# Optimization experiments

Measured on AMD Instinct MI355X. Metric: run time of the kernel, lower is better.

The kernel has to match this reference:

```python
import jax, jax.numpy as jnp
import numpy as np

# Hardcoded 6-node part graph from the module (src, dst) pairs; PyG flows src->dst.
_EDGES = np.array([[0,1],[0,2],[0,3],[0,4],[0,5],[1,2],[1,3],[1,4],[1,5],[2,3],[2,4],[3,5],[4,5],[1,0],[2,0],[3,0],[4,0],[5,0],[2,1],[3,1],[4,1],[5,1],[3,2],[4,2],[5,3],[5,4]], dtype=np.int32)
SRC = jnp.asarray(_EDGES[:, 0])
DST = jnp.asarray(_EDGES[:, 1])
NUM_NODES = 6


def setup_inputs() -> dict:
    key = jax.random.key(0)
    k0, k1, k2 = jax.random.split(key, 3)
    C, B = 128, 32768
    x = jax.random.normal(k0, (NUM_NODES, B, C), dtype=jnp.float32)
    # SAGEConv weights: lin_l (aggregated neighbors, carries bias) and lin_r (root)
    W_l = jax.random.normal(k1, (2 * C, C), dtype=jnp.float32) / np.sqrt(C).astype(np.float32)
    W_r = jax.random.normal(k2, (2 * C, C), dtype=jnp.float32) / np.sqrt(C).astype(np.float32)
    b = jnp.zeros((2 * C,), dtype=jnp.float32)
    return {"x": x, "W_l": W_l, "W_r": W_r, "b": b}


def reference(x, W_l, W_r, b):
    # x: [N=6, B, C]
    # mean aggregation of source features at each destination node
    msg = x[SRC]                                                  # [E, B, C]
    agg = jax.ops.segment_sum(msg, DST, num_segments=NUM_NODES)   # [N, B, C]
    deg = jax.ops.segment_sum(jnp.ones_like(DST, dtype=x.dtype), DST, num_segments=NUM_NODES)
    agg = agg / deg[:, None, None]
    # SAGEConv: lin_l(agg) + lin_r(x), bias in lin_l
    y = jnp.einsum('nbc,oc->nbo', agg, W_l) + b + jnp.einsum('nbc,oc->nbo', x, W_r)
    y = jax.nn.gelu(y, approximate=False)                         # torch F.gelu = exact erf
    # Python cat-loop over nodes == concatenate the 6 node slices along features
    N, B, O = y.shape
    return jnp.transpose(y, (1, 0, 2)).reshape(B, N * O)          # [B, 6*2C]
```

## Files before the change

kernel.cpp:

```cpp
#include <hip/hip_runtime.h>
#include <hip/hip_bf16.h>

#define NB 32768
#define CD 128
#define NNODES 6
#define OUTW 1536
#define GPB 8
#define NBLK (NB / 16 / GPB)

#define PW_P  0
#define PW_M0 32768
#define PW_M2 65536
#define PW_N  98304

typedef __attribute__((ext_vector_type(8))) short short8;
typedef __attribute__((ext_vector_type(4))) short s16x4;
typedef __attribute__((ext_vector_type(4))) float f32x4;

static __device__ __forceinline__ short f2bf(float f) {
    union { __bf16 b; short s; } u;
    u.b = (__bf16)f;
    return u.s;
}

static __device__ __forceinline__ short8 pack8(f32x4 a, f32x4 b) {
    short8 p;
    #pragma unroll
    for (int j = 0; j < 4; ++j) { p[j] = f2bf(a[j]); p[4 + j] = f2bf(b[j]); }
    return p;
}

static __device__ __forceinline__ s16x4 pack4(f32x4 a) {
    s16x4 p;
    #pragma unroll
    for (int j = 0; j < 4; ++j) p[j] = f2bf(a[j]);
    return p;
}

__global__ void prep_w(const float* __restrict__ Wl, const float* __restrict__ Wr,
                       short* __restrict__ Wb) {
    const int i = (blockIdx.x * 256 + threadIdx.x) * 8;
    const int o = i >> 7;
    const int k = i & 127;
    f32x4 l0 = *(const f32x4*)(Wl + o * CD + k);
    f32x4 l1 = *(const f32x4*)(Wl + o * CD + k + 4);
    f32x4 r0 = *(const f32x4*)(Wr + o * CD + k);
    f32x4 r1 = *(const f32x4*)(Wr + o * CD + k + 4);
    *(short8*)(Wb + PW_P  + i) = pack8(l0, l1);
    *(short8*)(Wb + PW_M0 + i) = pack8(r0 - 0.2f  * l0, r1 - 0.2f  * l1);
    *(short8*)(Wb + PW_M2 + i) = pack8(r0 - 0.25f * l0, r1 - 0.25f * l1);
    *(short8*)(Wb + PW_N  + i) = pack8(-0.25f * l0, -0.25f * l1);
}

#define LIDX(p, r, k) ((((p) << 11) + ((r) << 7) + (k)) ^ (((r) & 7) << 3))

__global__ __launch_bounds__(512, 1)
void sage_v16(const float* __restrict__ x, const short* __restrict__ Wb,
              const float* __restrict__ bias, float* __restrict__ out) {
    __shared__ __align__(16) float raw[2][NNODES * 16 * 128];
    __shared__ __align__(16) short A[7 * 16 * 128];

    const int t = threadIdx.x;
    const int r = t >> 5;
    const int c = t & 31;
    const int lane = t & 63;
    const int wv = t >> 6;
    const int lo = lane & 15;
    const int hi = lane >> 4;
    const int obase = wv * 32;
    const size_t rg0 = (size_t)blockIdx.x * GPB;

    f32x4 bias4[2];
    #pragma unroll
    for (int i = 0; i < 2; ++i)
        bias4[i] = *(const f32x4*)&bias[obase + i * 16 + hi * 4];

    auto stage = [&](int buf, size_t rg) {
        const float* gp = x + (rg * 16 + r) * CD + c * 4;
        #pragma unroll
        for (int s = 0; s < NNODES; ++s) {
            __builtin_amdgcn_global_load_lds(
                (const __attribute__((address_space(1))) void*)(gp + (size_t)s * (NB * CD)),
                (__attribute__((address_space(3))) void*)&raw[buf][s * 2048 + wv * 256],
                16, 0, 0);
        }
    };

    auto convert = [&](int buf) {
        const float* rb = &raw[buf][0];
        const int base = r * 128 + c * 4;
        f32x4 v0 = *(const f32x4*)&rb[0 * 2048 + base];
        f32x4 v1 = *(const f32x4*)&rb[1 * 2048 + base];
        f32x4 v2 = *(const f32x4*)&rb[2 * 2048 + base];
        f32x4 v3 = *(const f32x4*)&rb[3 * 2048 + base];
        f32x4 v4 = *(const f32x4*)&rb[4 * 2048 + base];
        f32x4 v5 = *(const f32x4*)&rb[5 * 2048 + base];
        f32x4 T = ((v0 + v1) + (v2 + v3)) + (v4 + v5);
        const int k = c * 4;
        *(s16x4*)&A[LIDX(0, r, k)] = pack4(v0);
        *(s16x4*)&A[LIDX(1, r, k)] = pack4(v1);
        *(s16x4*)&A[LIDX(2, r, k)] = pack4(v2);
        *(s16x4*)&A[LIDX(3, r, k)] = pack4(v3);
        *(s16x4*)&A[LIDX(4, r, k)] = pack4(v4);
        *(s16x4*)&A[LIDX(5, r, k)] = pack4(v5);
        *(s16x4*)&A[LIDX(6, r, k)] = pack4(T);
    };

    auto storePair = [&](int n0, int n1, f32x4 acc[2][2], size_t orow) {
        #pragma unroll
        for (int w = 0; w < 2; ++w) {
            const int node = w ? n1 : n0;
            #pragma unroll
            for (int i = 0; i < 2; ++i) {
                const int ocol = obase + i * 16 + hi * 4;
                f32x4 v = acc[w][i] + bias4[i];
                f32x4 g;
                #pragma unroll
                for (int j = 0; j < 4; ++j) {
                    const float s = v[j] * (0.7978845608f + 0.0356774081f * v[j] * v[j]);
                    const float rr = __builtin_amdgcn_exp2f(-2.885390082f * s);
                    g[j] = v[j] * __builtin_amdgcn_rcpf(1.0f + rr);
                }
                *(f32x4*)&out[orow * OUTW + node * 256 + ocol] = g;
            }
        }
    };

    stage(0, rg0);
    __syncthreads();
    convert(0);
    __syncthreads();

    f32x4 accH[2][2];
    size_t prevRow = 0;

    #pragma unroll 1
    for (int it = 0; it < GPB; ++it) {
        const bool havenext = (it + 1 < GPB);
        const size_t orow = (rg0 + it) * 16 + lo;

        if (havenext) stage((it + 1) & 1, rg0 + it + 1);
        if (it) storePair(3, 4, accH, prevRow);

        f32x4 accU[2] = {(f32x4){0.f,0.f,0.f,0.f}, (f32x4){0.f,0.f,0.f,0.f}};
        #pragma unroll
        for (int m = 0; m < 4; ++m) {
            const int kk = m * 32 + hi * 8;
            short8 ft = *(const short8*)&A[LIDX(6, lo, kk)];
            #pragma unroll
            for (int i = 0; i < 2; ++i) {
                const int o = obase + i * 16 + lo;
                short8 wp = *(const short8*)&Wb[PW_P + o * CD + kk];
                accU[i] = __builtin_amdgcn_mfma_f32_16x16x32_bf16(wp, ft, accU[i], 0, 0, 0);
            }
        }

        f32x4 acc[2][2];
        #pragma unroll
        for (int n = 0; n < 2; ++n)
            #pragma unroll
            for (int i = 0; i < 2; ++i) acc[n][i] = (f32x4){0.f,0.f,0.f,0.f};
        #pragma unroll
        for (int m = 0; m < 4; ++m) {
            const int kk = m * 32 + hi * 8;
            short8 f0 = *(const short8*)&A[LIDX(0, lo, kk)];
            short8 f1 = *(const short8*)&A[LIDX(1, lo, kk)];
            #pragma unroll
            for (int i = 0; i < 2; ++i) {
                const int o = obase + i * 16 + lo;
                short8 wm = *(const short8*)&Wb[PW_M0 + o * CD + kk];
                acc[0][i] = __builtin_amdgcn_mfma_f32_16x16x32_bf16(wm, f0, acc[0][i], 0, 0, 0);
                acc[1][i] = __builtin_amdgcn_mfma_f32_16x16x32_bf16(wm, f1, acc[1][i], 0, 0, 0);
            }
        }
        #pragma unroll
        for (int n = 0; n < 2; ++n)
            #pragma unroll
            for (int i = 0; i < 2; ++i) acc[n][i] += 0.2f * accU[i];
        storePair(0, 1, acc, orow);

        #pragma unroll
        for (int n = 0; n < 2; ++n)
            #pragma unroll
            for (int i = 0; i < 2; ++i) acc[n][i] = (f32x4){0.f,0.f,0.f,0.f};
        #pragma unroll
        for (int m = 0; m < 4; ++m) {
            const int kk = m * 32 + hi * 8;
            short8 fa = *(const short8*)&A[LIDX(2, lo, kk)];
            short8 fb = *(const short8*)&A[LIDX(5, lo, kk)];
            #pragma unroll
            for (int i = 0; i < 2; ++i) {
                const int o = obase + i * 16 + lo;
                short8 wm = *(const short8*)&Wb[PW_M2 + o * CD + kk];
                short8 wn = *(const short8*)&Wb[PW_N  + o * CD + kk];
                acc[0][i] = __builtin_amdgcn_mfma_f32_16x16x32_bf16(wm, fa, acc[0][i], 0, 0, 0);
                acc[0][i] = __builtin_amdgcn_mfma_f32_16x16x32_bf16(wn, fb, acc[0][i], 0, 0, 0);
                acc[1][i] = __builtin_amdgcn_mfma_f32_16x16x32_bf16(wm, fb, acc[1][i], 0, 0, 0);
                acc[1][i] = __builtin_amdgcn_mfma_f32_16x16x32_bf16(wn, fa, acc[1][i], 0, 0, 0);
            }
        }
        #pragma unroll
        for (int n = 0; n < 2; ++n)
            #pragma unroll
            for (int i = 0; i < 2; ++i) acc[n][i] += 0.25f * accU[i];
        storePair(2, 5, acc, orow);

        #pragma unroll
        for (int n = 0; n < 2; ++n)
            #pragma unroll
            for (int i = 0; i < 2; ++i) accH[n][i] = (f32x4){0.f,0.f,0.f,0.f};
        #pragma unroll
        for (int m = 0; m < 4; ++m) {
            const int kk = m * 32 + hi * 8;
            short8 fa = *(const short8*)&A[LIDX(3, lo, kk)];
            short8 fb = *(const short8*)&A[LIDX(4, lo, kk)];
            #pragma unroll
            for (int i = 0; i < 2; ++i) {
                const int o = obase + i * 16 + lo;
                short8 wm = *(const short8*)&Wb[PW_M2 + o * CD + kk];
                short8 wn = *(const short8*)&Wb[PW_N  + o * CD + kk];
                accH[0][i] = __builtin_amdgcn_mfma_f32_16x16x32_bf16(wm, fa, accH[0][i], 0, 0, 0);
                accH[0][i] = __builtin_amdgcn_mfma_f32_16x16x32_bf16(wn, fb, accH[0][i], 0, 0, 0);
                accH[1][i] = __builtin_amdgcn_mfma_f32_16x16x32_bf16(wm, fb, accH[1][i], 0, 0, 0);
                accH[1][i] = __builtin_amdgcn_mfma_f32_16x16x32_bf16(wn, fa, accH[1][i], 0, 0, 0);
            }
        }
        #pragma unroll
        for (int n = 0; n < 2; ++n)
            #pragma unroll
            for (int i = 0; i < 2; ++i) accH[n][i] += 0.25f * accU[i];
        prevRow = orow;

        __syncthreads();
        if (havenext) convert((it + 1) & 1);
        __syncthreads();
    }
    storePair(3, 4, accH, prevRow);
}

extern "C" void kernel_launch(void* const* d_in, const int* in_sizes, int n_in,
                              void* d_out, int out_size, void* d_ws, size_t ws_size,
                              hipStream_t stream) {
    const float* x  = (const float*)d_in[0];
    const float* Wl = (const float*)d_in[1];
    const float* Wr = (const float*)d_in[2];
    const float* b  = (const float*)d_in[3];
    float* out = (float*)d_out;
    short* Wb = (short*)d_ws;

    prep_w<<<dim3(16), dim3(256), 0, stream>>>(Wl, Wr, Wb);
    sage_v16<<<dim3(NBLK), dim3(512), 0, stream>>>(x, Wb, b, out);
}
```

Baseline: 88.83 us.

## Warp-specialize into producer and MFMA consumer waves with deeper prefetch

```diff
diff --git a/kernel.cpp b/kernel.cpp
--- a/kernel.cpp
+++ b/kernel.cpp
@@ -3,7 +3,6 @@
 
 #define NB 32768
 #define CD 128
-#define NNODES 6
 #define OUTW 1536
 #define GPB 8
 #define NBLK (NB / 16 / GPB)
@@ -14,7 +13,6 @@
 #define PW_N  98304
 
 typedef __attribute__((ext_vector_type(8))) short short8;
-typedef __attribute__((ext_vector_type(4))) short s16x4;
 typedef __attribute__((ext_vector_type(4))) float f32x4;
 
 static __device__ __forceinline__ short f2bf(float f) {
@@ -27,13 +25,6 @@
     short8 p;
     #pragma unroll
     for (int j = 0; j < 4; ++j) { p[j] = f2bf(a[j]); p[4 + j] = f2bf(b[j]); }
-    return p;
-}
-
-static __device__ __forceinline__ s16x4 pack4(f32x4 a) {
-    s16x4 p;
-    #pragma unroll
-    for (int j = 0; j < 4; ++j) p[j] = f2bf(a[j]);
     return p;
 }
 
@@ -55,63 +46,71 @@
 #define LIDX(p, r, k) ((((p) << 11) + ((r) << 7) + (k)) ^ (((r) & 7) << 3))
 
 __global__ __launch_bounds__(512, 1)
-void sage_v16(const float* __restrict__ x, const short* __restrict__ Wb,
+void sage_v19(const float* __restrict__ x, const short* __restrict__ Wb,
               const float* __restrict__ bias, float* __restrict__ out) {
-    __shared__ __align__(16) float raw[2][NNODES * 16 * 128];
-    __shared__ __align__(16) short A[7 * 16 * 128];
+    __shared__ __align__(16) float raw[2][6 * 16 * 128];
+    __shared__ __align__(16) short A[2][7 * 16 * 128];
 
     const int t = threadIdx.x;
-    const int r = t >> 5;
-    const int c = t & 31;
     const int lane = t & 63;
     const int wv = t >> 6;
     const int lo = lane & 15;
     const int hi = lane >> 4;
-    const int obase = wv * 32;
     const size_t rg0 = (size_t)blockIdx.x * GPB;
 
-    f32x4 bias4[2];
-    #pragma unroll
-    for (int i = 0; i < 2; ++i)
-        bias4[i] = *(const f32x4*)&bias[obase + i * 16 + hi * 4];
-
     auto stage = [&](int buf, size_t rg) {
-        const float* gp = x + (rg * 16 + r) * CD + c * 4;
-        #pragma unroll
-        for (int s = 0; s < NNODES; ++s) {
-            __builtin_amdgcn_global_load_lds(
-                (const __attribute__((address_space(1))) void*)(gp + (size_t)s * (NB * CD)),
-                (__attribute__((address_space(3))) void*)&raw[buf][s * 2048 + wv * 256],
-                16, 0, 0);
-        }
-    };
-
+        const int q = wv - 4;
+        const size_t gbase = rg * 16 * CD;
+        #pragma unroll
+        for (int s = 0; s < 6; ++s)
+            #pragma unroll
+            for (int j = 0; j < 2; ++j) {
+                const int off = (q * 2 + j) * 256;
+                __builtin_amdgcn_global_load_lds(
+                    (const __attribute__((address_space(1))) void*)
+                        (x + (size_t)s * (NB * CD) + gbase + off + (lane << 2)),
+                    (__attribute__((address_space(3))) void*)&raw[buf][s * 2048 + off],
+                    16, 0, 0);
+            }
+    };
     auto convert = [&](int buf) {
+        const int u = t & 255;
+        const int r = u >> 4;
+        const int c = u & 15;
         const float* rb = &raw[buf][0];
-        const int base = r * 128 + c * 4;
-        f32x4 v0 = *(const f32x4*)&rb[0 * 2048 + base];
-        f32x4 v1 = *(const f32x4*)&rb[1 * 2048 + base];
-        f32x4 v2 = *(const f32x4*)&rb[2 * 2048 + base];
-        f32x4 v3 = *(const f32x4*)&rb[3 * 2048 + base];
-        f32x4 v4 = *(const f32x4*)&rb[4 * 2048 + base];
-        f32x4 v5 = *(const f32x4*)&rb[5 * 2048 + base];
-        f32x4 T = ((v0 + v1) + (v2 + v3)) + (v4 + v5);
-        const int k = c * 4;
-        *(s16x4*)&A[LIDX(0, r, k)] = pack4(v0);
-        *(s16x4*)&A[LIDX(1, r, k)] = pack4(v1);
-        *(s16x4*)&A[LIDX(2, r, k)] = pack4(v2);
-        *(s16x4*)&A[LIDX(3, r, k)] = pack4(v3);
-        *(s16x4*)&A[LIDX(4, r, k)] = pack4(v4);
-        *(s16x4*)&A[LIDX(5, r, k)] = pack4(v5);
-        *(s16x4*)&A[LIDX(6, r, k)] = pack4(T);
-    };
-
-    auto storePair = [&](int n0, int n1, f32x4 acc[2][2], size_t orow) {
+        const int base = r * 128 + c * 8;
+        f32x4 a0 = *(const f32x4*)&rb[0 * 2048 + base], b0 = *(const f32x4*)&rb[0 * 2048 + base + 4];
+        f32x4 a1 = *(const f32x4*)&rb[1 * 2048 + base], b1 = *(const f32x4*)&rb[1 * 2048 + base + 4];
+        f32x4 a2 = *(const f32x4*)&rb[2 * 2048 + base], b2 = *(const f32x4*)&rb[2 * 2048 + base + 4];
+        f32x4 a3 = *(const f32x4*)&rb[3 * 2048 + base], b3 = *(const f32x4*)&rb[3 * 2048 + base + 4];
+        f32x4 a4 = *(const f32x4*)&rb[4 * 2048 + base], b4 = *(const f32x4*)&rb[4 * 2048 + base + 4];
+        f32x4 a5 = *(const f32x4*)&rb[5 * 2048 + base], b5 = *(const f32x4*)&rb[5 * 2048 + base + 4];
+        f32x4 Ta = ((a0 + a1) + (a2 + a3)) + (a4 + a5);
+        f32x4 Tb = ((b0 + b1) + (b2 + b3)) + (b4 + b5);
+        short* Ad = &A[buf][0];
+        const int k = c * 8;
+        *(short8*)&Ad[LIDX(0, r, k)] = pack8(a0, b0);
+        *(short8*)&Ad[LIDX(1, r, k)] = pack8(a1, b1);
+        *(short8*)&Ad[LIDX(2, r, k)] = pack8(a2, b2);
+        *(short8*)&Ad[LIDX(3, r, k)] = pack8(a3, b3);
+        *(short8*)&Ad[LIDX(4, r, k)] = pack8(a4, b4);
+        *(short8*)&Ad[LIDX(5, r, k)] = pack8(a5, b5);
+        *(short8*)&Ad[LIDX(6, r, k)] = pack8(Ta, Tb);
+    };
+
+    const int obase = wv * 64;
+    f32x4 bias4[4];
+    if (wv < 4) {
+        #pragma unroll
+        for (int i = 0; i < 4; ++i)
+            bias4[i] = *(const f32x4*)&bias[obase + i * 16 + hi * 4];
+    }
+    auto storePair = [&](int n0, int n1, f32x4 acc[2][4], size_t orow) {
         #pragma unroll
         for (int w = 0; w < 2; ++w) {
             const int node = w ? n1 : n0;
             #pragma unroll
-            for (int i = 0; i < 2; ++i) {
+            for (int i = 0; i < 4; ++i) {
                 const int ocol = obase + i * 16 + hi * 4;
                 f32x4 v = acc[w][i] + bias4[i];
                 f32x4 g;
@@ -125,117 +124,105 @@
             }
         }
     };
-
-    stage(0, rg0);
-    __syncthreads();
-    convert(0);
-    __syncthreads();
-
-    f32x4 accH[2][2];
+    auto pairMFMA = [&](const short* Ab, int p0, int p1, int mOwn, int mN,
+                        f32x4 acc[2][4]) {
+        #pragma unroll
+        for (int n = 0; n < 2; ++n)
+            #pragma unroll
+            for (int i = 0; i < 4; ++i) acc[n][i] = (f32x4){0.f,0.f,0.f,0.f};
+        __builtin_amdgcn_s_setprio(1);
+        #pragma unroll
+        for (int m = 0; m < 4; ++m) {
+            const int kk = m * 32 + hi * 8;
+            short8 fa = *(const short8*)&Ab[LIDX(p0, lo, kk)];
+            short8 fb = *(const short8*)&Ab[LIDX(p1, lo, kk)];
+            #pragma unroll
+            for (int i = 0; i < 4; ++i) {
+                const int widx = (obase + i * 16 + lo) * CD + kk;
+                short8 wm = *(const short8*)&Wb[mOwn + widx];
+                acc[0][i] = __builtin_amdgcn_mfma_f32_16x16x32_bf16(wm, fa, acc[0][i], 0, 0, 0);
+                acc[1][i] = __builtin_amdgcn_mfma_f32_16x16x32_bf16(wm, fb, acc[1][i], 0, 0, 0);
+                if (mN >= 0) {
+                    short8 wn = *(const short8*)&Wb[mN + widx];
+                    acc[0][i] = __builtin_amdgcn_mfma_f32_16x16x32_bf16(wn, fb, acc[0][i], 0, 0, 0);
+                    acc[1][i] = __builtin_amdgcn_mfma_f32_16x16x32_bf16(wn, fa, acc[1][i], 0, 0, 0);
+                }
+            }
+        }
+        __builtin_amdgcn_s_setprio(0);
+    };
+
+    if (wv >= 4) {
+        stage(0, rg0);
+        asm volatile("s_waitcnt vmcnt(0)" ::: "memory");
+        convert(0);
+        if (GPB > 1) stage(1, rg0 + 1);
+    }
+    asm volatile("s_waitcnt lgkmcnt(0)" ::: "memory");
+    __builtin_amdgcn_s_barrier();
+
+    f32x4 accH[2][4];
     size_t prevRow = 0;
 
     #pragma unroll 1
     for (int it = 0; it < GPB; ++it) {
-        const bool havenext = (it + 1 < GPB);
-        const size_t orow = (rg0 + it) * 16 + lo;
-
-        if (havenext) stage((it + 1) & 1, rg0 + it + 1);
-        if (it) storePair(3, 4, accH, prevRow);
-
-        f32x4 accU[2] = {(f32x4){0.f,0.f,0.f,0.f}, (f32x4){0.f,0.f,0.f,0.f}};
-        #pragma unroll
-        for (int m = 0; m < 4; ++m) {
-            const int kk = m * 32 + hi * 8;
-            short8 ft = *(const short8*)&A[LIDX(6, lo, kk)];
-            #pragma unroll
-            for (int i = 0; i < 2; ++i) {
-                const int o = obase + i * 16 + lo;
-                short8 wp = *(const short8*)&Wb[PW_P + o * CD + kk];
-                accU[i] = __builtin_amdgcn_mfma_f32_16x16x32_bf16(wp, ft, accU[i], 0, 0, 0);
+        if (wv < 4) {
+            const short* Ab = &A[it & 1][0];
+            const size_t orow = (rg0 + it) * 16 + lo;
+            if (it) storePair(3, 4, accH, prevRow);
+
+            f32x4 accU[4];
+            #pragma unroll
+            for (int i = 0; i < 4; ++i) accU[i] = (f32x4){0.f,0.f,0.f,0.f};
+            __builtin_amdgcn_s_setprio(1);
+            #pragma unroll
+            for (int m = 0; m < 4; ++m) {
+                const int kk = m * 32 + hi * 8;
+                short8 ft = *(const short8*)&Ab[LIDX(6, lo, kk)];
+                #pragma unroll
+                for (int i = 0; i < 4; ++i) {
+                    short8 wp = *(const short8*)&Wb[PW_P + (obase + i * 16 + lo) * CD + kk];
+                    accU[i] = __builtin_amdgcn_mfma_f32_16x16x32_bf16(wp, ft, accU[i], 0, 0, 0);
+                }
+            }
+            __builtin_amdgcn_s_setprio(0);
+
+            f32x4 acc[2][4];
+            pairMFMA(Ab, 0, 1, PW_M0, -1, acc);
+            #pragma unroll
+            for (int n = 0; n < 2; ++n)
+                #pragma unroll
+                for (int i = 0; i < 4; ++i) acc[n][i] += 0.2f * accU[i];
+            storePair(0, 1, acc, orow);
+
+            pairMFMA(Ab, 2, 5, PW_M2, PW_N, acc);
+            #pragma unroll
+            for (int n = 0; n < 2; ++n)
+                #pragma unroll
+                for (int i = 0; i < 4; ++i) acc[n][i] += 0.25f * accU[i];
+            storePair(2, 5, acc, orow);
+
+            pairMFMA(Ab, 3, 4, PW_M2, PW_N, accH);
+            #pragma unroll
+            for (int n = 0; n < 2; ++n)
+                #pragma unroll
+                for (int i = 0; i < 4; ++i) accH[n][i] += 0.25f * accU[i];
+            prevRow = orow;
+        } else {
+            if (it + 1 < GPB) {
+                if (it + 2 < GPB) {
+                    stage(it & 1, rg0 + it + 2);
+                    asm volatile("s_waitcnt vmcnt(12)" ::: "memory");
+                } else {
+                    asm volatile("s_waitcnt vmcnt(0)" ::: "memory");
+                }
+                convert((it + 1) & 1);
             }
         }
-
-        f32x4 acc[2][2];
-        #pragma unroll
-        for (int n = 0; n < 2; ++n)
-            #pragma unroll
-            for (int i = 0; i < 2; ++i) acc[n][i] = (f32x4){0.f,0.f,0.f,0.f};
-        #pragma unroll
-        for (int m = 0; m < 4; ++m) {
-            const int kk = m * 32 + hi * 8;
-            short8 f0 = *(const short8*)&A[LIDX(0, lo, kk)];
-            short8 f1 = *(const short8*)&A[LIDX(1, lo, kk)];
-            #pragma unroll
-            for (int i = 0; i < 2; ++i) {
-                const int o = obase + i * 16 + lo;
-                short8 wm = *(const short8*)&Wb[PW_M0 + o * CD + kk];
-                acc[0][i] = __builtin_amdgcn_mfma_f32_16x16x32_bf16(wm, f0, acc[0][i], 0, 0, 0);
-                acc[1][i] = __builtin_amdgcn_mfma_f32_16x16x32_bf16(wm, f1, acc[1][i], 0, 0, 0);
-            }
-        }
-        #pragma unroll
-        for (int n = 0; n < 2; ++n)
-            #pragma unroll
-            for (int i = 0; i < 2; ++i) acc[n][i] += 0.2f * accU[i];
-        storePair(0, 1, acc, orow);
-
-        #pragma unroll
-        for (int n = 0; n < 2; ++n)
-            #pragma unroll
-            for (int i = 0; i < 2; ++i) acc[n][i] = (f32x4){0.f,0.f,0.f,0.f};
-        #pragma unroll
-        for (int m = 0; m < 4; ++m) {
-            const int kk = m * 32 + hi * 8;
-            short8 fa = *(const short8*)&A[LIDX(2, lo, kk)];
-            short8 fb = *(const short8*)&A[LIDX(5, lo, kk)];
-            #pragma unroll
-            for (int i = 0; i < 2; ++i) {
-                const int o = obase + i * 16 + lo;
-                short8 wm = *(const short8*)&Wb[PW_M2 + o * CD + kk];
-                short8 wn = *(const short8*)&Wb[PW_N  + o * CD + kk];
-                acc[0][i] = __builtin_amdgcn_mfma_f32_16x16x32_bf16(wm, fa, acc[0][i], 0, 0, 0);
-                acc[0][i] = __builtin_amdgcn_mfma_f32_16x16x32_bf16(wn, fb, acc[0][i], 0, 0, 0);
-                acc[1][i] = __builtin_amdgcn_mfma_f32_16x16x32_bf16(wm, fb, acc[1][i], 0, 0, 0);
-                acc[1][i] = __builtin_amdgcn_mfma_f32_16x16x32_bf16(wn, fa, acc[1][i], 0, 0, 0);
-            }
-        }
-        #pragma unroll
-        for (int n = 0; n < 2; ++n)
-            #pragma unroll
-            for (int i = 0; i < 2; ++i) acc[n][i] += 0.25f * accU[i];
-        storePair(2, 5, acc, orow);
-
-        #pragma unroll
-        for (int n = 0; n < 2; ++n)
-            #pragma unroll
-            for (int i = 0; i < 2; ++i) accH[n][i] = (f32x4){0.f,0.f,0.f,0.f};
-        #pragma unroll
-        for (int m = 0; m < 4; ++m) {
-            const int kk = m * 32 + hi * 8;
-            short8 fa = *(const short8*)&A[LIDX(3, lo, kk)];
-            short8 fb = *(const short8*)&A[LIDX(4, lo, kk)];
-            #pragma unroll
-            for (int i = 0; i < 2; ++i) {
-                const int o = obase + i * 16 + lo;
-                short8 wm = *(const short8*)&Wb[PW_M2 + o * CD + kk];
-                short8 wn = *(const short8*)&Wb[PW_N  + o * CD + kk];
-                accH[0][i] = __builtin_amdgcn_mfma_f32_16x16x32_bf16(wm, fa, accH[0][i], 0, 0, 0);
-                accH[0][i] = __builtin_amdgcn_mfma_f32_16x16x32_bf16(wn, fb, accH[0][i], 0, 0, 0);
-                accH[1][i] = __builtin_amdgcn_mfma_f32_16x16x32_bf16(wm, fb, accH[1][i], 0, 0, 0);
-                accH[1][i] = __builtin_amdgcn_mfma_f32_16x16x32_bf16(wn, fa, accH[1][i], 0, 0, 0);
-            }
-        }
-        #pragma unroll
-        for (int n = 0; n < 2; ++n)
-            #pragma unroll
-            for (int i = 0; i < 2; ++i) accH[n][i] += 0.25f * accU[i];
-        prevRow = orow;
-
-        __syncthreads();
-        if (havenext) convert((it + 1) & 1);
-        __syncthreads();
+        asm volatile("s_waitcnt lgkmcnt(0)" ::: "memory");
+        __builtin_amdgcn_s_barrier();
     }
-    storePair(3, 4, accH, prevRow);
+    if (wv < 4) storePair(3, 4, accH, prevRow);
 }
 
 extern "C" void kernel_launch(void* const* d_in, const int* in_sizes, int n_in,
@@ -249,5 +236,5 @@
     short* Wb = (short*)d_ws;
 
     prep_w<<<dim3(16), dim3(256), 0, stream>>>(Wl, Wr, Wb);
-    sage_v16<<<dim3(NBLK), dim3(512), 0, stream>>>(x, Wb, b, out);
-}
+    sage_v19<<<dim3(NBLK), dim3(512), 0, stream>>>(x, Wb, b, out);
+}
```

Result: slower. 191.3 us (+115.4%).
